# Kernel optimization log

Measured on AMD Instinct MI355X. Metric: run time of the kernel, lower is better.

The kernel has to match this reference:

```python
import jax, jax.numpy as jnp
import numpy as np

B, C, H, W = 32, 512, 64, 64
P = 8            # partition (window) size
HEAD_DIM = 32
N_HEADS = C // HEAD_DIM  # 16
MLP_RATIO = 4
LN_EPS = 1e-5


def _rel_pos_index(p):
    # Swin/MaxViT-style relative position index for a p x p window -> [p*p, p*p]
    coords = np.stack(np.meshgrid(np.arange(p), np.arange(p), indexing='ij'), 0).reshape(2, -1)
    rel = coords[:, :, None] - coords[:, None, :]          # [2, pp, pp]
    rel = rel.transpose(1, 2, 0) + (p - 1)                 # shift to >= 0
    idx = rel[..., 0] * (2 * p - 1) + rel[..., 1]          # [pp, pp]
    return jnp.asarray(idx, jnp.int32)


def setup_inputs() -> dict:
    key = jax.random.key(0)
    ks = jax.random.split(key, 10)
    s = 0.02
    d_ff = MLP_RATIO * C
    inp = {
        'x': jax.random.normal(ks[0], (B, C, H, W), jnp.float32),
        'gamma1': jnp.ones((C,), jnp.float32),
        'beta1': jnp.zeros((C,), jnp.float32),
        'gamma2': jnp.ones((C,), jnp.float32),
        'beta2': jnp.zeros((C,), jnp.float32),
        'qkv_w': jax.random.normal(ks[1], (C, 3 * C), jnp.float32) * s,
        'qkv_b': jnp.zeros((3 * C,), jnp.float32),
        'merge_w': jax.random.normal(ks[2], (C, C), jnp.float32) * s,
        'merge_b': jnp.zeros((C,), jnp.float32),
        'bias_table': jax.random.normal(ks[3], ((2 * P - 1) ** 2, N_HEADS), jnp.float32) * s,
        'w1': jax.random.normal(ks[4], (C, d_ff), jnp.float32) * s,
        'b1': jnp.zeros((d_ff,), jnp.float32),
        'w2': jax.random.normal(ks[5], (d_ff, C), jnp.float32) * s,
        'b2': jnp.zeros((C,), jnp.float32),
        'rel_idx': _rel_pos_index(P),
    }
    return inp


def _layernorm(t, g, b):
    mu = jnp.mean(t, axis=-1, keepdims=True)
    var = jnp.mean(jnp.square(t - mu), axis=-1, keepdims=True)
    return (t - mu) * jax.lax.rsqrt(var + LN_EPS) * g + b


def reference(x, gamma1, beta1, gamma2, beta2, qkv_w, qkv_b, merge_w, merge_b,
              bias_table, w1, b1, w2, b2, rel_idx):
    p, hd, nh = P, HEAD_DIM, N_HEADS
    Bx, Cx, Hx, Wx = x.shape
    hp, wp = Hx // p, Wx // p
    G, PP = hp * wp, p * p

    # --- window partition: [B,C,H,W] -> [B, G, p*p, C] (partition_type='window', no swap)
    xw = x.reshape(Bx, Cx, hp, p, wp, p).transpose(0, 2, 4, 3, 5, 1).reshape(Bx, G, PP, Cx)

    # --- relative-position multi-head attention on norm1(x)
    h = _layernorm(xw, gamma1, beta1)
    qkv = h @ qkv_w + qkv_b                                   # [B,G,PP,3C]
    q, k, v = jnp.split(qkv, 3, axis=-1)
    q = q.reshape(Bx, G, PP, nh, hd) * (hd ** -0.5)
    k = k.reshape(Bx, G, PP, nh, hd)
    v = v.reshape(Bx, G, PP, nh, hd)
    attn = jnp.einsum('bgqhd,bgkhd->bghqk', q, k)             # [B,G,nh,PP,PP]
    bias = bias_table[rel_idx]                                # [PP,PP,nh]
    attn = attn + bias.transpose(2, 0, 1)[None, None]
    attn = jax.nn.softmax(attn, axis=-1)
    o = jnp.einsum('bghqk,bgkhd->bgqhd', attn, v).reshape(Bx, G, PP, Cx)
    xw = xw + (o @ merge_w + merge_b)                          # residual (dropout/SD p=0)

    # --- MLP block on norm2(x)
    h2 = _layernorm(xw, gamma2, beta2)
    m = jax.nn.gelu(h2 @ w1 + b1) @ w2 + b2
    xw = xw + m

    # --- window departition: [B,G,p*p,C] -> [B,C,H,W]
    out = xw.reshape(Bx, hp, wp, p, p, Cx).transpose(0, 5, 1, 3, 2, 4).reshape(Bx, Cx, Hx, Wx)
    return out
```

## Files before the change

kernel.cpp:

```cpp
#include <hip/hip_runtime.h>
#include <stdint.h>

typedef __attribute__((ext_vector_type(8))) short short8;
typedef __attribute__((ext_vector_type(4))) float f32x4;
typedef __attribute__((address_space(3))) void lds_void;
typedef __attribute__((address_space(1))) void gv_void;

static __device__ __forceinline__ float bf2f(unsigned short u) {
    union { uint32_t i; float f; } v; v.i = ((uint32_t)u) << 16; return v.f;
}
static __device__ __forceinline__ unsigned short f2bf(float f) {
    union { float f; uint32_t i; } v; v.f = f;
    uint32_t i = v.i;
    uint32_t r = (i + 0x7fffu + ((i >> 16) & 1u)) >> 16;
    return (unsigned short)r;
}
static __device__ __forceinline__ float fexp(float x) {
    float r;
    asm("v_exp_f32 %0, %1" : "=v"(r) : "v"(x * 1.44269504088896f));
    return r;
}
static __device__ __forceinline__ float frcp(float x) {
    float r;
    asm("v_rcp_f32 %0, %1" : "=v"(r) : "v"(x));
    return r;
}

__global__ void k_detect(const void* __restrict__ g1, int* __restrict__ flag) {
    if (threadIdx.x == 0 && blockIdx.x == 0) {
        const unsigned short* u = (const unsigned short*)g1;
        flag[0] = (u[0] == 0x3F80u) ? 0 : 1;
    }
}

__global__ __launch_bounds__(256) void k_cvt(const void* __restrict__ src,
                                             unsigned short* __restrict__ dst,
                                             int n, const int* __restrict__ flag) {
    int i = blockIdx.x * 256 + threadIdx.x;
    if (i < n) {
        dst[i] = flag[0] ? f2bf(((const float*)src)[i])
                         : ((const unsigned short*)src)[i];
    }
}

__global__ __launch_bounds__(256) void k_transpose(const void* __restrict__ in,
                                                   unsigned short* __restrict__ out,
                                                   int R, int C, const int* __restrict__ flag) {
    __shared__ unsigned short tile[32][33];
    int isf = flag[0];
    int tx = threadIdx.x, ty = threadIdx.y;
    int x = blockIdx.x * 32 + tx;
    int y0 = blockIdx.y * 32;
    for (int j = ty; j < 32; j += 8) {
        size_t idx = (size_t)(y0 + j) * C + x;
        tile[j][tx] = isf ? f2bf(((const float*)in)[idx]) : ((const unsigned short*)in)[idx];
    }
    __syncthreads();
    int x2 = y0 + tx;
    int y20 = blockIdx.x * 32;
    for (int j = ty; j < 32; j += 8)
        out[(size_t)(y20 + j) * R + x2] = tile[tx][j];
}

__global__ __launch_bounds__(256) void k_prep_bias(const void* __restrict__ bias_table,
                                                   const int* __restrict__ rel_idx,
                                                   float* __restrict__ biasp,
                                                   const int* __restrict__ flag) {
    int i = blockIdx.x * 256 + threadIdx.x;
    int isf = flag[0];
    int h = i & 15, qk = i >> 4;
    size_t idx = (size_t)rel_idx[qk] * 16 + h;
    float v = isf ? ((const float*)bias_table)[idx] : bf2f(((const unsigned short*)bias_table)[idx]);
    biasp[h * 4096 + qk] = v;
}

__global__ __launch_bounds__(256) void k_partition_ln(const void* __restrict__ x,
                                                      const unsigned short* __restrict__ g1,
                                                      const unsigned short* __restrict__ b1,
                                                      unsigned short* __restrict__ xw,
                                                      unsigned short* __restrict__ h,
                                                      int b0, const int* __restrict__ flag) {
    __shared__ unsigned short tile[64][512];
    int isf = flag[0];
    int bh = blockIdx.x, bl = bh >> 6, hh = bh & 63;
    int b = b0 + bl;
    int tid = threadIdx.x;
    size_t xoff = (((size_t)b * 512) * 64 + hh) * 64;
    int c0 = tid >> 3, ch = tid & 7;
    if (isf) {
        const float* xb = (const float*)x + xoff;
        for (int k = 0; k < 16; ++k) {
            int c = c0 + k * 32;
            f32x4 v0 = *reinterpret_cast<const f32x4*>(xb + (size_t)c * 4096 + ch * 8);
            f32x4 v1 = *reinterpret_cast<const f32x4*>(xb + (size_t)c * 4096 + ch * 8 + 4);
#pragma unroll
            for (int j = 0; j < 4; ++j) tile[ch * 8 + j][c] = f2bf(v0[j]);
#pragma unroll
            for (int j = 0; j < 4; ++j) tile[ch * 8 + 4 + j][c] = f2bf(v1[j]);
        }
    } else {
        const unsigned short* xb = (const unsigned short*)x + xoff;
        for (int k = 0; k < 16; ++k) {
            int c = c0 + k * 32;
            short8 v = *reinterpret_cast<const short8*>(xb + (size_t)c * 4096 + ch * 8);
#pragma unroll
            for (int j = 0; j < 8; ++j) tile[ch * 8 + j][c] = (unsigned short)v[j];
        }
    }
    __syncthreads();
    int w = tid >> 2, q = tid & 3;
    float s = 0.f, s2 = 0.f;
#pragma unroll 4
    for (int j = 0; j < 128; ++j) {
        int c = q * 128 + ((j + 8 * w) & 127);
        float f = bf2f(tile[w][c]);
        s += f; s2 += f * f;
    }
    s += __shfl_xor(s, 1);  s += __shfl_xor(s, 2);
    s2 += __shfl_xor(s2, 1); s2 += __shfl_xor(s2, 2);
    float mu = s * (1.f / 512.f);
    float rstd = rsqrtf(s2 * (1.f / 512.f) - mu * mu + 1e-5f);
    int t = (bl * 64 + (hh >> 3) * 8 + (w >> 3)) * 64 + (hh & 7) * 8 + (w & 7);
    unsigned short* xr = xw + (size_t)t * 512;
    unsigned short* hr = h + (size_t)t * 512;
    for (int cc = q * 128; cc < q * 128 + 128; cc += 8) {
        short8 raw, hn;
#pragma unroll
        for (int j = 0; j < 8; ++j) {
            unsigned short u = tile[w][cc + j];
            raw[j] = (short)u;
            float f = (bf2f(u) - mu) * rstd * bf2f(g1[cc + j]) + bf2f(b1[cc + j]);
            hn[j] = (short)f2bf(f);
        }
        *reinterpret_cast<short8*>(xr + cc) = raw;
        *reinterpret_cast<short8*>(hr + cc) = hn;
    }
}

__global__ __launch_bounds__(256) void k_ln(const unsigned short* __restrict__ in,
                                            const unsigned short* __restrict__ g,
                                            const unsigned short* __restrict__ b,
                                            unsigned short* __restrict__ out) {
    int wid = threadIdx.x >> 6, lane = threadIdx.x & 63;
    size_t t = (size_t)blockIdx.x * 4 + wid;
    short8 v = *reinterpret_cast<const short8*>(in + t * 512 + lane * 8);
    float f[8], s = 0.f, s2 = 0.f;
#pragma unroll
    for (int j = 0; j < 8; ++j) { f[j] = bf2f((unsigned short)v[j]); s += f[j]; s2 += f[j] * f[j]; }
    for (int m = 1; m < 64; m <<= 1) { s += __shfl_xor(s, m); s2 += __shfl_xor(s2, m); }
    float mu = s * (1.f / 512.f);
    float rstd = rsqrtf(s2 * (1.f / 512.f) - mu * mu + 1e-5f);
    short8 ov;
#pragma unroll
    for (int j = 0; j < 8; ++j)
        ov[j] = (short)f2bf((f[j] - mu) * rstd * bf2f(g[lane * 8 + j]) + bf2f(b[lane * 8 + j]));
    *reinterpret_cast<short8*>(out + t * 512 + lane * 8) = ov;
}

template <int MODE>
__global__ __launch_bounds__(512, 1) void k_gemm5(const unsigned short* __restrict__ A,
                                                  const unsigned short* __restrict__ BT,
                                                  const unsigned short* __restrict__ bias,
                                                  const unsigned short* __restrict__ res,
                                                  unsigned short* __restrict__ out,
                                                  int M, int N, int K) {
    __shared__ unsigned short S[65536];
    const int tid = threadIdx.x, lane = tid & 63, wid = tid >> 6;

    int nwg = gridDim.x * gridDim.y;
    int lin = blockIdx.y * gridDim.x + blockIdx.x;
    int swz = (lin & 7) * (nwg >> 3) + (lin >> 3);
    int mt = swz % gridDim.x, nt = swz / gridDim.x;

    const int wr = wid >> 2, wc = wid & 3;
    const int rl = lane & 15, qg = lane >> 4;

    const int strow = tid >> 2;
    const int scb   = (tid & 3) ^ ((tid >> 3) & 3);
    const unsigned short* Agb = A  + ((size_t)mt * 256 + strow) * K + scb * 8;
    const unsigned short* Bgb = BT + ((size_t)nt * 256 + strow) * K + scb * 8;
    const int ldst = strow * 32 + (tid & 3) * 8;

    f32x4 acc[8][4];
#pragma unroll
    for (int mf = 0; mf < 8; ++mf)
#pragma unroll
        for (int nf = 0; nf < 4; ++nf) {
            acc[mf][nf][0] = 0.f; acc[mf][nf][1] = 0.f; acc[mf][nf][2] = 0.f; acc[mf][nf][3] = 0.f;
        }

    const int NH = K >> 5;

    auto stage = [&](int h) {
        int base = (h & 3) * 16384;
#pragma unroll
        for (int s = 0; s < 2; ++s) {
            __builtin_amdgcn_global_load_lds((const gv_void*)(Agb + (size_t)s * 128 * K + h * 32),
                                             (lds_void*)(&S[base + s * 4096 + ldst]), 16, 0, 0);
            __builtin_amdgcn_global_load_lds((const gv_void*)(Bgb + (size_t)s * 128 * K + h * 32),
                                             (lds_void*)(&S[base + 8192 + s * 4096 + ldst]), 16, 0, 0);
        }
    };

    stage(0); stage(1); stage(2);

    const int arow0 = wr * 128 + rl;
    const int brow0 = wc * 64 + rl;
    const int kbr = (qg ^ ((rl >> 1) & 3)) * 8;

    for (int h = 0; h < NH; ++h) {
        const unsigned short* sA = &S[(h & 3) * 16384];
        const unsigned short* sB = sA + 8192;
        if (h + 3 < NH) {
            stage(h + 3);
            asm volatile("s_waitcnt vmcnt(12)" ::: "memory");
        } else if (h + 2 < NH) {
            asm volatile("s_waitcnt vmcnt(8)" ::: "memory");
        } else if (h + 1 < NH) {
            asm volatile("s_waitcnt vmcnt(4)" ::: "memory");
        } else {
            asm volatile("s_waitcnt vmcnt(0)" ::: "memory");
        }
        __builtin_amdgcn_s_barrier();
        asm volatile("" ::: "memory");

        short8 af[8], bfr[4];
#pragma unroll
        for (int nf = 0; nf < 4; ++nf)
            bfr[nf] = *reinterpret_cast<const short8*>(&sB[(brow0 + nf * 16) * 32 + kbr]);
#pragma unroll
        for (int mf = 0; mf < 8; ++mf)
            af[mf] = *reinterpret_cast<const short8*>(&sA[(arow0 + mf * 16) * 32 + kbr]);

        __builtin_amdgcn_s_setprio(1);
#pragma unroll
        for (int mf = 0; mf < 8; ++mf)
#pragma unroll
            for (int nf = 0; nf < 4; ++nf)
                acc[mf][nf] = __builtin_amdgcn_mfma_f32_16x16x32_bf16(af[mf], bfr[nf], acc[mf][nf], 0, 0, 0);
        __builtin_amdgcn_s_setprio(0);

        __builtin_amdgcn_s_barrier();
        asm volatile("" ::: "memory");
    }

    const int PST = 264;
    unsigned short* pb = (unsigned short*)S;
    float bz[4];
#pragma unroll
    for (int nf = 0; nf < 4; ++nf) bz[nf] = bf2f(bias[nt * 256 + wc * 64 + nf * 16 + rl]);
    int row_l = tid >> 4, cbl = (tid & 15) * 16;
    int growb = mt * 256 + (row_l >> 4) * 128 + (row_l & 15);
    size_t gcol = (size_t)nt * 256 + cbl;

#pragma unroll
    for (int mf = 0; mf < 8; ++mf) {
        __syncthreads();
#pragma unroll
        for (int nf = 0; nf < 4; ++nf)
#pragma unroll
            for (int r = 0; r < 4; ++r) {
                float v = acc[mf][nf][r] + bz[nf];
                if (MODE == 2) {
                    float z = 0.7978845608f * (v + 0.044715f * v * v * v);
                    float e = fexp(-2.0f * z);
                    v = v * frcp(1.f + e);
                }
                pb[(wr * 16 + qg * 4 + r) * PST + wc * 64 + nf * 16 + rl] = f2bf(v);
            }
        __syncthreads();
        size_t go = (size_t)(growb + mf * 16) * N + gcol;
        short8 o1 = *reinterpret_cast<const short8*>(&pb[row_l * PST + cbl]);
        short8 o2 = *reinterpret_cast<const short8*>(&pb[row_l * PST + cbl + 8]);
        if (MODE == 1) {
            short8 r1 = *reinterpret_cast<const short8*>(&res[go]);
            short8 r2 = *reinterpret_cast<const short8*>(&res[go + 8]);
#pragma unroll
            for (int j = 0; j < 8; ++j) {
                o1[j] = (short)f2bf(bf2f((unsigned short)o1[j]) + bf2f((unsigned short)r1[j]));
                o2[j] = (short)f2bf(bf2f((unsigned short)o2[j]) + bf2f((unsigned short)r2[j]));
            }
        }
        *reinterpret_cast<short8*>(&out[go]) = o1;
        *reinterpret_cast<short8*>(&out[go + 8]) = o2;
    }
}

__global__ __launch_bounds__(64) void k_attn(const unsigned short* __restrict__ qkv,
                                             const float* __restrict__ biasp,
                                             unsigned short* __restrict__ o) {
    __shared__ unsigned short Pl[64][72];
    int blk = blockIdx.x;
    int head = blk & 15, win = blk >> 4;
    size_t T0 = (size_t)win * 64;
    int lane = threadIdx.x;
    int rl = lane & 15, qg = lane >> 4;
    const unsigned short* base = qkv + T0 * 1536;
    int qoff = head * 32, koff = 512 + head * 32, voff = 1024 + head * 32;

    f32x4 s[4][4];
#pragma unroll
    for (int m = 0; m < 4; ++m)
#pragma unroll
        for (int n = 0; n < 4; ++n) { s[m][n][0] = 0.f; s[m][n][1] = 0.f; s[m][n][2] = 0.f; s[m][n][3] = 0.f; }

    short8 aq[4], bk[4];
#pragma unroll
    for (int m = 0; m < 4; ++m)
        aq[m] = *reinterpret_cast<const short8*>(base + (size_t)(16 * m + rl) * 1536 + qoff + qg * 8);
#pragma unroll
    for (int n = 0; n < 4; ++n)
        bk[n] = *reinterpret_cast<const short8*>(base + (size_t)(16 * n + rl) * 1536 + koff + qg * 8);
#pragma unroll
    for (int m = 0; m < 4; ++m)
#pragma unroll
        for (int n = 0; n < 4; ++n)
            s[m][n] = __builtin_amdgcn_mfma_f32_16x16x32_bf16(aq[m], bk[n], s[m][n], 0, 0, 0);

    const float scale = 0.17677669529663687f;
    const float* bh = biasp + head * 4096;
#pragma unroll
    for (int m = 0; m < 4; ++m) {
#pragma unroll
        for (int r = 0; r < 4; ++r) {
            int row = 16 * m + qg * 4 + r;
            float v0 = s[m][0][r] * scale + bh[row * 64 + rl];
            float v1 = s[m][1][r] * scale + bh[row * 64 + 16 + rl];
            float v2 = s[m][2][r] * scale + bh[row * 64 + 32 + rl];
            float v3 = s[m][3][r] * scale + bh[row * 64 + 48 + rl];
            float mx = fmaxf(fmaxf(v0, v1), fmaxf(v2, v3));
            mx = fmaxf(mx, __shfl_xor(mx, 1));
            mx = fmaxf(mx, __shfl_xor(mx, 2));
            mx = fmaxf(mx, __shfl_xor(mx, 4));
            mx = fmaxf(mx, __shfl_xor(mx, 8));
            v0 = fexp(v0 - mx); v1 = fexp(v1 - mx); v2 = fexp(v2 - mx); v3 = fexp(v3 - mx);
            float sm = v0 + v1 + v2 + v3;
            sm += __shfl_xor(sm, 1);
            sm += __shfl_xor(sm, 2);
            sm += __shfl_xor(sm, 4);
            sm += __shfl_xor(sm, 8);
            float inv = frcp(sm);
            Pl[row][rl]      = f2bf(v0 * inv);
            Pl[row][16 + rl] = f2bf(v1 * inv);
            Pl[row][32 + rl] = f2bf(v2 * inv);
            Pl[row][48 + rl] = f2bf(v3 * inv);
        }
    }
    __syncthreads();

    short8 bv[2][2];
#pragma unroll
    for (int ks = 0; ks < 2; ++ks)
#pragma unroll
        for (int n2 = 0; n2 < 2; ++n2) {
            short8 t;
#pragma unroll
            for (int i = 0; i < 8; ++i)
                t[i] = (short)base[(size_t)(32 * ks + qg * 8 + i) * 1536 + voff + n2 * 16 + rl];
            bv[ks][n2] = t;
        }

    f32x4 acc2[4][2];
#pragma unroll
    for (int m = 0; m < 4; ++m)
#pragma unroll
        for (int n2 = 0; n2 < 2; ++n2) { acc2[m][n2][0] = 0.f; acc2[m][n2][1] = 0.f; acc2[m][n2][2] = 0.f; acc2[m][n2][3] = 0.f; }

#pragma unroll
    for (int m = 0; m < 4; ++m) {
        short8 p0 = *reinterpret_cast<const short8*>(&Pl[16 * m + rl][qg * 8]);
        short8 p1 = *reinterpret_cast<const short8*>(&Pl[16 * m + rl][32 + qg * 8]);
#pragma unroll
        for (int n2 = 0; n2 < 2; ++n2) {
            acc2[m][n2] = __builtin_amdgcn_mfma_f32_16x16x32_bf16(p0, bv[0][n2], acc2[m][n2], 0, 0, 0);
            acc2[m][n2] = __builtin_amdgcn_mfma_f32_16x16x32_bf16(p1, bv[1][n2], acc2[m][n2], 0, 0, 0);
        }
    }
#pragma unroll
    for (int m = 0; m < 4; ++m)
#pragma unroll
        for (int n2 = 0; n2 < 2; ++n2)
#pragma unroll
            for (int r = 0; r < 4; ++r) {
                int row = 16 * m + qg * 4 + r;
                o[(T0 + row) * 512 + head * 32 + n2 * 16 + rl] = f2bf(acc2[m][n2][r]);
            }
}

__global__ __launch_bounds__(256) void k_departition(const unsigned short* __restrict__ tok,
                                                     void* __restrict__ xo,
                                                     int b0, const int* __restrict__ flag) {
    __shared__ unsigned short tile[64][512];
    int isf = flag[0];
    int bh = blockIdx.x, bl = bh >> 6, hh = bh & 63;
    int b = b0 + bl;
    int tid = threadIdx.x;
    int Tb = (bl * 64 + (hh >> 3) * 8) * 64 + (hh & 7) * 8;
    for (int k = 0; k < 16; ++k) {
        int flat = k * 256 + tid;
        int w = flat >> 6, ch = flat & 63;
        int t = Tb + (w >> 3) * 64 + (w & 7);
        short8 v = *reinterpret_cast<const short8*>(tok + (size_t)t * 512 + ch * 8);
        *reinterpret_cast<short8*>(&tile[w][ch * 8]) = v;
    }
    __syncthreads();
    size_t xoff = (((size_t)b * 512) * 64 + hh) * 64;
    if (isf) {
        float* xb = (float*)xo + xoff;
        for (int k = 0; k < 16; ++k) {
            int flat = k * 256 + tid;
            int c = flat >> 3, wc = flat & 7;
            f32x4 a, d;
#pragma unroll
            for (int j = 0; j < 4; ++j) a[j] = bf2f(tile[wc * 8 + j][c]);
#pragma unroll
            for (int j = 0; j < 4; ++j) d[j] = bf2f(tile[wc * 8 + 4 + j][c]);
            *reinterpret_cast<f32x4*>(xb + (size_t)c * 4096 + wc * 8) = a;
            *reinterpret_cast<f32x4*>(xb + (size_t)c * 4096 + wc * 8 + 4) = d;
        }
    } else {
        unsigned short* xb = (unsigned short*)xo + xoff;
        for (int k = 0; k < 16; ++k) {
            int flat = k * 256 + tid;
            int c = flat >> 3, wc = flat & 7;
            short8 v;
#pragma unroll
            for (int j = 0; j < 8; ++j) v[j] = (short)tile[wc * 8 + j][c];
            *reinterpret_cast<short8*>(xb + (size_t)c * 4096 + wc * 8) = v;
        }
    }
}

extern "C" void kernel_launch(void* const* d_in, const int* in_sizes, int n_in,
                              void* d_out, int out_size, void* d_ws, size_t ws_size,
                              hipStream_t stream) {
    const void* x          = d_in[0];
    const void* g1         = d_in[1];
    const void* be1        = d_in[2];
    const void* g2         = d_in[3];
    const void* be2        = d_in[4];
    const void* qkv_w      = d_in[5];
    const void* qkv_b      = d_in[6];
    const void* merge_w    = d_in[7];
    const void* merge_b    = d_in[8];
    const void* bias_table = d_in[9];
    const void* w1         = d_in[10];
    const void* b1         = d_in[11];
    const void* w2         = d_in[12];
    const void* b2         = d_in[13];
    const int*  rel_idx    = (const int*)d_in[14];

    const size_t extra = 8u << 20;
    int CB = 4;
    if (ws_size >= (size_t)32768 * 10240 + extra) CB = 8;
    int nch = 32 / CB;
    size_t tok = (size_t)CB * 4096;

    unsigned short* xw_c     = (unsigned short*)d_ws;
    unsigned short* h_c      = xw_c + tok * 512;
    unsigned short* o_c      = h_c + tok * 512;
    unsigned short* qkv_c    = o_c + tok * 512;
    unsigned short* mid_c    = qkv_c + tok * 1536;
    unsigned short* qkv_wT   = mid_c + tok * 2048;
    unsigned short* merge_wT = qkv_wT + 1536 * 512;
    unsigned short* w1T      = merge_wT + 512 * 512;
    unsigned short* w2T      = w1T + 2048 * 512;
    unsigned short* vecs     = w2T + 512 * 2048;
    float*          biasp    = (float*)(vecs + 6656);
    int*            flag     = (int*)(biasp + 65536);

    unsigned short* ng1 = vecs + 0,    *nbe1 = vecs + 512;
    unsigned short* ng2 = vecs + 1024, *nbe2 = vecs + 1536;
    unsigned short* nqb = vecs + 2048, *nmb  = vecs + 3584;
    unsigned short* nb1 = vecs + 4096, *nb2  = vecs + 6144;

    k_detect<<<1, 64, 0, stream>>>(g1, flag);
    k_cvt<<<2, 256, 0, stream>>>(g1, ng1, 512, flag);
    k_cvt<<<2, 256, 0, stream>>>(be1, nbe1, 512, flag);
    k_cvt<<<2, 256, 0, stream>>>(g2, ng2, 512, flag);
    k_cvt<<<2, 256, 0, stream>>>(be2, nbe2, 512, flag);
    k_cvt<<<6, 256, 0, stream>>>(qkv_b, nqb, 1536, flag);
    k_cvt<<<2, 256, 0, stream>>>(merge_b, nmb, 512, flag);
    k_cvt<<<8, 256, 0, stream>>>(b1, nb1, 2048, flag);
    k_cvt<<<2, 256, 0, stream>>>(b2, nb2, 512, flag);
    k_transpose<<<dim3(48, 16), dim3(32, 8), 0, stream>>>(qkv_w, qkv_wT, 512, 1536, flag);
    k_transpose<<<dim3(16, 16), dim3(32, 8), 0, stream>>>(merge_w, merge_wT, 512, 512, flag);
    k_transpose<<<dim3(64, 16), dim3(32, 8), 0, stream>>>(w1, w1T, 512, 2048, flag);
    k_transpose<<<dim3(16, 64), dim3(32, 8), 0, stream>>>(w2, w2T, 2048, 512, flag);
    k_prep_bias<<<256, 256, 0, stream>>>(bias_table, rel_idx, biasp, flag);

    int mtiles = (int)(tok / 256);
    int M = (int)tok;
    for (int c = 0; c < nch; ++c) {
        int b0 = c * CB;
        k_partition_ln<<<CB * 64, 256, 0, stream>>>(x, ng1, nbe1, xw_c, h_c, b0, flag);
        k_gemm5<0><<<dim3(mtiles, 6), 512, 0, stream>>>(h_c, qkv_wT, nqb, nullptr, qkv_c, M, 1536, 512);
        k_attn<<<CB * 1024, 64, 0, stream>>>(qkv_c, biasp, o_c);
        k_gemm5<1><<<dim3(mtiles, 2), 512, 0, stream>>>(o_c, merge_wT, nmb, xw_c, xw_c, M, 512, 512);
        k_ln<<<(int)(tok / 4), 256, 0, stream>>>(xw_c, ng2, nbe2, h_c);
        k_gemm5<2><<<dim3(mtiles, 8), 512, 0, stream>>>(h_c, w1T, nb1, nullptr, mid_c, M, 2048, 512);
        k_gemm5<1><<<dim3(mtiles, 2), 512, 0, stream>>>(mid_c, w2T, nb2, xw_c, qkv_c, M, 512, 2048);
        k_departition<<<CB * 64, 256, 0, stream>>>(qkv_c, d_out, b0, flag);
    }
}
```

Baseline: 1.870 ms.

## Fuse departition into FFN2 epilogue and emit transposed V from QKV GEMM

Measured after the change: 1.964 ms. +5.0%, slower.

```diff
diff --git a/kernel.cpp b/kernel.cpp
--- a/kernel.cpp
+++ b/kernel.cpp
@@ -23,6 +23,11 @@
 static __device__ __forceinline__ float frcp(float x) {
     float r;
     asm("v_rcp_f32 %0, %1" : "=v"(r) : "v"(x));
+    return r;
+}
+static __device__ __forceinline__ uint32_t cvtpk(float lo, float hi) {
+    uint32_t r;
+    asm("v_cvt_pk_bf16_f32 %0, %1, %2" : "=v"(r) : "v"(lo), "v"(hi));
     return r;
 }
 
@@ -64,14 +69,16 @@
 
 __global__ __launch_bounds__(256) void k_prep_bias(const void* __restrict__ bias_table,
                                                    const int* __restrict__ rel_idx,
-                                                   float* __restrict__ biasp,
+                                                   float* __restrict__ biasb,
                                                    const int* __restrict__ flag) {
     int i = blockIdx.x * 256 + threadIdx.x;
     int isf = flag[0];
-    int h = i & 15, qk = i >> 4;
-    size_t idx = (size_t)rel_idx[qk] * 16 + h;
+    int r  = i & 3, rl = (i >> 2) & 15, qg = (i >> 6) & 3;
+    int km = (i >> 8) & 3, qn = (i >> 10) & 3, h = (i >> 12) & 15;
+    int q = 16 * qn + rl, k = 16 * km + 4 * qg + r;
+    size_t idx = (size_t)rel_idx[q * 64 + k] * 16 + h;
     float v = isf ? ((const float*)bias_table)[idx] : bf2f(((const unsigned short*)bias_table)[idx]);
-    biasp[h * 4096 + qk] = v;
+    biasb[i] = v;
 }
 
 __global__ __launch_bounds__(256) void k_partition_ln(const void* __restrict__ x,
@@ -158,11 +165,14 @@
 }
 
 template <int MODE>
-__global__ __launch_bounds__(512, 1) void k_gemm5(const unsigned short* __restrict__ A,
+__global__ __launch_bounds__(512, 1) void k_gemm6(const unsigned short* __restrict__ A,
                                                   const unsigned short* __restrict__ BT,
                                                   const unsigned short* __restrict__ bias,
                                                   const unsigned short* __restrict__ res,
                                                   unsigned short* __restrict__ out,
+                                                  unsigned short* __restrict__ vt,
+                                                  void* __restrict__ outx,
+                                                  int b0, const int* __restrict__ flag,
                                                   int M, int N, int K) {
     __shared__ unsigned short S[65536];
     const int tid = threadIdx.x, lane = tid & 63, wid = tid >> 6;
@@ -252,6 +262,7 @@
     int row_l = tid >> 4, cbl = (tid & 15) * 16;
     int growb = mt * 256 + (row_l >> 4) * 128 + (row_l & 15);
     size_t gcol = (size_t)nt * 256 + cbl;
+    const int isf = (MODE == 3) ? flag[0] : 0;
 
 #pragma unroll
     for (int mf = 0; mf < 8; ++mf) {
@@ -266,169 +277,170 @@
                     float e = fexp(-2.0f * z);
                     v = v * frcp(1.f + e);
                 }
+                if (MODE == 3) {
+                    size_t rowg = (size_t)(mt * 256 + wr * 128 + mf * 16 + qg * 4 + r);
+                    v += bf2f(res[rowg * N + nt * 256 + wc * 64 + nf * 16 + rl]);
+                }
                 pb[(wr * 16 + qg * 4 + r) * PST + wc * 64 + nf * 16 + rl] = f2bf(v);
             }
         __syncthreads();
-        size_t go = (size_t)(growb + mf * 16) * N + gcol;
-        short8 o1 = *reinterpret_cast<const short8*>(&pb[row_l * PST + cbl]);
-        short8 o2 = *reinterpret_cast<const short8*>(&pb[row_l * PST + cbl + 8]);
-        if (MODE == 1) {
-            short8 r1 = *reinterpret_cast<const short8*>(&res[go]);
-            short8 r2 = *reinterpret_cast<const short8*>(&res[go + 8]);
-#pragma unroll
-            for (int j = 0; j < 8; ++j) {
-                o1[j] = (short)f2bf(bf2f((unsigned short)o1[j]) + bf2f((unsigned short)r1[j]));
-                o2[j] = (short)f2bf(bf2f((unsigned short)o2[j]) + bf2f((unsigned short)r2[j]));
+
+        if (MODE == 0 && nt >= 4) {
+#pragma unroll
+            for (int s = 0; s < 2; ++s) {
+                int run = tid + 512 * s;
+                int c = run & 255, hp = run >> 8, half = hp >> 1, ph = hp & 1;
+                int prow = half * 16 + ph * 8;
+                short8 v8;
+#pragma unroll
+                for (int i = 0; i < 8; ++i) v8[i] = (short)pb[(prow + i) * PST + c];
+                int t0 = mt * 256 + half * 128 + mf * 16 + ph * 8;
+                int cc = nt * 256 + c - 1024;
+                int win = t0 >> 6, k0 = t0 & 63;
+                *reinterpret_cast<short8*>(&vt[((size_t)(win * 16 + (cc >> 5)) * 32 + (cc & 31)) * 64 + k0]) = v8;
             }
-        }
-        *reinterpret_cast<short8*>(&out[go]) = o1;
-        *reinterpret_cast<short8*>(&out[go + 8]) = o2;
-    }
-}
-
-__global__ __launch_bounds__(64) void k_attn(const unsigned short* __restrict__ qkv,
-                                             const float* __restrict__ biasp,
-                                             unsigned short* __restrict__ o) {
-    __shared__ unsigned short Pl[64][72];
+        } else if (MODE == 3) {
+#pragma unroll
+            for (int s = 0; s < 2; ++s) {
+                int run = tid + 512 * s;
+                int c = run & 255, hp = run >> 8, half = hp >> 1, ph = hp & 1;
+                int prow = half * 16 + ph * 8;
+                int t0 = mt * 256 + half * 128 + mf * 16 + ph * 8;
+                int ch = nt * 256 + c;
+                int b = b0 + (t0 >> 12), win = (t0 >> 6) & 63, py = (t0 >> 3) & 7;
+                size_t xoff = ((size_t)(b * 512 + ch)) * 4096 + ((win >> 3) * 8 + py) * 64 + (win & 7) * 8;
+                if (isf) {
+                    f32x4 a, d;
+#pragma unroll
+                    for (int i = 0; i < 4; ++i) a[i] = bf2f(pb[(prow + i) * PST + c]);
+#pragma unroll
+                    for (int i = 0; i < 4; ++i) d[i] = bf2f(pb[(prow + 4 + i) * PST + c]);
+                    *reinterpret_cast<f32x4*>((float*)outx + xoff) = a;
+                    *reinterpret_cast<f32x4*>((float*)outx + xoff + 4) = d;
+                } else {
+                    short8 v8;
+#pragma unroll
+                    for (int i = 0; i < 8; ++i) v8[i] = (short)pb[(prow + i) * PST + c];
+                    *reinterpret_cast<short8*>((unsigned short*)outx + xoff) = v8;
+                }
+            }
+        } else {
+            size_t go = (size_t)(growb + mf * 16) * N + gcol;
+            short8 o1 = *reinterpret_cast<const short8*>(&pb[row_l * PST + cbl]);
+            short8 o2 = *reinterpret_cast<const short8*>(&pb[row_l * PST + cbl + 8]);
+            if (MODE == 1) {
+                short8 r1 = *reinterpret_cast<const short8*>(&res[go]);
+                short8 r2 = *reinterpret_cast<const short8*>(&res[go + 8]);
+#pragma unroll
+                for (int j = 0; j < 8; ++j) {
+                    o1[j] = (short)f2bf(bf2f((unsigned short)o1[j]) + bf2f((unsigned short)r1[j]));
+                    o2[j] = (short)f2bf(bf2f((unsigned short)o2[j]) + bf2f((unsigned short)r2[j]));
+                }
+            }
+            *reinterpret_cast<short8*>(&out[go]) = o1;
+            *reinterpret_cast<short8*>(&out[go + 8]) = o2;
+        }
+    }
+}
+
+__global__ __launch_bounds__(64) void k_attn2(const unsigned short* __restrict__ qkv,
+                                              const unsigned short* __restrict__ vt,
+                                              const float* __restrict__ biasb,
+                                              unsigned short* __restrict__ o) {
+    __shared__ unsigned short Pl[64 * 72];
     int blk = blockIdx.x;
     int head = blk & 15, win = blk >> 4;
     size_t T0 = (size_t)win * 64;
     int lane = threadIdx.x;
     int rl = lane & 15, qg = lane >> 4;
     const unsigned short* base = qkv + T0 * 1536;
-    int qoff = head * 32, koff = 512 + head * 32, voff = 1024 + head * 32;
-
-    f32x4 s[4][4];
-#pragma unroll
-    for (int m = 0; m < 4; ++m)
-#pragma unroll
-        for (int n = 0; n < 4; ++n) { s[m][n][0] = 0.f; s[m][n][1] = 0.f; s[m][n][2] = 0.f; s[m][n][3] = 0.f; }
-
-    short8 aq[4], bk[4];
-#pragma unroll
-    for (int m = 0; m < 4; ++m)
-        aq[m] = *reinterpret_cast<const short8*>(base + (size_t)(16 * m + rl) * 1536 + qoff + qg * 8);
-#pragma unroll
-    for (int n = 0; n < 4; ++n)
-        bk[n] = *reinterpret_cast<const short8*>(base + (size_t)(16 * n + rl) * 1536 + koff + qg * 8);
-#pragma unroll
-    for (int m = 0; m < 4; ++m)
-#pragma unroll
-        for (int n = 0; n < 4; ++n)
-            s[m][n] = __builtin_amdgcn_mfma_f32_16x16x32_bf16(aq[m], bk[n], s[m][n], 0, 0, 0);
+    int qoff = head * 32, koff = 512 + head * 32;
+
+    short8 kf[4], qf[4];
+#pragma unroll
+    for (int m = 0; m < 4; ++m) {
+        kf[m] = *reinterpret_cast<const short8*>(base + (size_t)(16 * m + rl) * 1536 + koff + qg * 8);
+        qf[m] = *reinterpret_cast<const short8*>(base + (size_t)(16 * m + rl) * 1536 + qoff + qg * 8);
+    }
+    f32x4 st[4][4];
+#pragma unroll
+    for (int km = 0; km < 4; ++km)
+#pragma unroll
+        for (int qn = 0; qn < 4; ++qn) { st[km][qn][0] = 0.f; st[km][qn][1] = 0.f; st[km][qn][2] = 0.f; st[km][qn][3] = 0.f; }
+#pragma unroll
+    for (int km = 0; km < 4; ++km)
+#pragma unroll
+        for (int qn = 0; qn < 4; ++qn)
+            st[km][qn] = __builtin_amdgcn_mfma_f32_16x16x32_bf16(kf[km], qf[qn], st[km][qn], 0, 0, 0);
 
     const float scale = 0.17677669529663687f;
-    const float* bh = biasp + head * 4096;
-#pragma unroll
-    for (int m = 0; m < 4; ++m) {
-#pragma unroll
-        for (int r = 0; r < 4; ++r) {
-            int row = 16 * m + qg * 4 + r;
-            float v0 = s[m][0][r] * scale + bh[row * 64 + rl];
-            float v1 = s[m][1][r] * scale + bh[row * 64 + 16 + rl];
-            float v2 = s[m][2][r] * scale + bh[row * 64 + 32 + rl];
-            float v3 = s[m][3][r] * scale + bh[row * 64 + 48 + rl];
-            float mx = fmaxf(fmaxf(v0, v1), fmaxf(v2, v3));
-            mx = fmaxf(mx, __shfl_xor(mx, 1));
-            mx = fmaxf(mx, __shfl_xor(mx, 2));
-            mx = fmaxf(mx, __shfl_xor(mx, 4));
-            mx = fmaxf(mx, __shfl_xor(mx, 8));
-            v0 = fexp(v0 - mx); v1 = fexp(v1 - mx); v2 = fexp(v2 - mx); v3 = fexp(v3 - mx);
-            float sm = v0 + v1 + v2 + v3;
-            sm += __shfl_xor(sm, 1);
-            sm += __shfl_xor(sm, 2);
-            sm += __shfl_xor(sm, 4);
-            sm += __shfl_xor(sm, 8);
-            float inv = frcp(sm);
-            Pl[row][rl]      = f2bf(v0 * inv);
-            Pl[row][16 + rl] = f2bf(v1 * inv);
-            Pl[row][32 + rl] = f2bf(v2 * inv);
-            Pl[row][48 + rl] = f2bf(v3 * inv);
-        }
-    }
+    const float* bh = biasb + head * 4096 + qg * 64 + rl * 4;
+#pragma unroll
+    for (int qn = 0; qn < 4; ++qn) {
+        float vv[4][4];
+        float mx = -3.0e38f;
+#pragma unroll
+        for (int km = 0; km < 4; ++km) {
+            f32x4 b4 = *reinterpret_cast<const f32x4*>(bh + qn * 1024 + km * 256);
+#pragma unroll
+            for (int r = 0; r < 4; ++r) {
+                vv[km][r] = st[km][qn][r] * scale + b4[r];
+                mx = fmaxf(mx, vv[km][r]);
+            }
+        }
+        mx = fmaxf(mx, __shfl_xor(mx, 16));
+        mx = fmaxf(mx, __shfl_xor(mx, 32));
+        float sm = 0.f;
+#pragma unroll
+        for (int km = 0; km < 4; ++km)
+#pragma unroll
+            for (int r = 0; r < 4; ++r) { vv[km][r] = fexp(vv[km][r] - mx); sm += vv[km][r]; }
+        sm += __shfl_xor(sm, 16);
+        sm += __shfl_xor(sm, 32);
+        float inv = frcp(sm);
+        int q = 16 * qn + rl;
+#pragma unroll
+        for (int km = 0; km < 4; ++km) {
+            uint32_t w0 = cvtpk(vv[km][0] * inv, vv[km][1] * inv);
+            uint32_t w1 = cvtpk(vv[km][2] * inv, vv[km][3] * inv);
+            uint32_t* p = reinterpret_cast<uint32_t*>(&Pl[q * 72 + 16 * km + 4 * qg]);
+            p[0] = w0; p[1] = w1;
+        }
+    }
+
+    short8 vf[2][2];
+    const unsigned short* vb = vt + (size_t)(win * 16 + head) * 2048;
+#pragma unroll
+    for (int kb = 0; kb < 2; ++kb)
+#pragma unroll
+        for (int dn = 0; dn < 2; ++dn)
+            vf[kb][dn] = *reinterpret_cast<const short8*>(vb + (16 * dn + rl) * 64 + 32 * kb + 8 * qg);
+
     __syncthreads();
 
-    short8 bv[2][2];
-#pragma unroll
-    for (int ks = 0; ks < 2; ++ks)
-#pragma unroll
-        for (int n2 = 0; n2 < 2; ++n2) {
-            short8 t;
-#pragma unroll
-            for (int i = 0; i < 8; ++i)
-                t[i] = (short)base[(size_t)(32 * ks + qg * 8 + i) * 1536 + voff + n2 * 16 + rl];
-            bv[ks][n2] = t;
-        }
-
-    f32x4 acc2[4][2];
-#pragma unroll
-    for (int m = 0; m < 4; ++m)
-#pragma unroll
-        for (int n2 = 0; n2 < 2; ++n2) { acc2[m][n2][0] = 0.f; acc2[m][n2][1] = 0.f; acc2[m][n2][2] = 0.f; acc2[m][n2][3] = 0.f; }
-
-#pragma unroll
-    for (int m = 0; m < 4; ++m) {
-        short8 p0 = *reinterpret_cast<const short8*>(&Pl[16 * m + rl][qg * 8]);
-        short8 p1 = *reinterpret_cast<const short8*>(&Pl[16 * m + rl][32 + qg * 8]);
-#pragma unroll
-        for (int n2 = 0; n2 < 2; ++n2) {
-            acc2[m][n2] = __builtin_amdgcn_mfma_f32_16x16x32_bf16(p0, bv[0][n2], acc2[m][n2], 0, 0, 0);
-            acc2[m][n2] = __builtin_amdgcn_mfma_f32_16x16x32_bf16(p1, bv[1][n2], acc2[m][n2], 0, 0, 0);
-        }
-    }
-#pragma unroll
-    for (int m = 0; m < 4; ++m)
-#pragma unroll
-        for (int n2 = 0; n2 < 2; ++n2)
-#pragma unroll
-            for (int r = 0; r < 4; ++r) {
-                int row = 16 * m + qg * 4 + r;
-                o[(T0 + row) * 512 + head * 32 + n2 * 16 + rl] = f2bf(acc2[m][n2][r]);
-            }
-}
-
-__global__ __launch_bounds__(256) void k_departition(const unsigned short* __restrict__ tok,
-                                                     void* __restrict__ xo,
-                                                     int b0, const int* __restrict__ flag) {
-    __shared__ unsigned short tile[64][512];
-    int isf = flag[0];
-    int bh = blockIdx.x, bl = bh >> 6, hh = bh & 63;
-    int b = b0 + bl;
-    int tid = threadIdx.x;
-    int Tb = (bl * 64 + (hh >> 3) * 8) * 64 + (hh & 7) * 8;
-    for (int k = 0; k < 16; ++k) {
-        int flat = k * 256 + tid;
-        int w = flat >> 6, ch = flat & 63;
-        int t = Tb + (w >> 3) * 64 + (w & 7);
-        short8 v = *reinterpret_cast<const short8*>(tok + (size_t)t * 512 + ch * 8);
-        *reinterpret_cast<short8*>(&tile[w][ch * 8]) = v;
-    }
-    __syncthreads();
-    size_t xoff = (((size_t)b * 512) * 64 + hh) * 64;
-    if (isf) {
-        float* xb = (float*)xo + xoff;
-        for (int k = 0; k < 16; ++k) {
-            int flat = k * 256 + tid;
-            int c = flat >> 3, wc = flat & 7;
-            f32x4 a, d;
-#pragma unroll
-            for (int j = 0; j < 4; ++j) a[j] = bf2f(tile[wc * 8 + j][c]);
-#pragma unroll
-            for (int j = 0; j < 4; ++j) d[j] = bf2f(tile[wc * 8 + 4 + j][c]);
-            *reinterpret_cast<f32x4*>(xb + (size_t)c * 4096 + wc * 8) = a;
-            *reinterpret_cast<f32x4*>(xb + (size_t)c * 4096 + wc * 8 + 4) = d;
-        }
-    } else {
-        unsigned short* xb = (unsigned short*)xo + xoff;
-        for (int k = 0; k < 16; ++k) {
-            int flat = k * 256 + tid;
-            int c = flat >> 3, wc = flat & 7;
-            short8 v;
-#pragma unroll
-            for (int j = 0; j < 8; ++j) v[j] = (short)tile[wc * 8 + j][c];
-            *reinterpret_cast<short8*>(xb + (size_t)c * 4096 + wc * 8) = v;
-        }
-    }
+    f32x4 acc[4][2];
+#pragma unroll
+    for (int qm = 0; qm < 4; ++qm)
+#pragma unroll
+        for (int dn = 0; dn < 2; ++dn) { acc[qm][dn][0] = 0.f; acc[qm][dn][1] = 0.f; acc[qm][dn][2] = 0.f; acc[qm][dn][3] = 0.f; }
+
+#pragma unroll
+    for (int qm = 0; qm < 4; ++qm) {
+        short8 a0 = *reinterpret_cast<const short8*>(&Pl[(16 * qm + rl) * 72 + 8 * qg]);
+        short8 a1 = *reinterpret_cast<const short8*>(&Pl[(16 * qm + rl) * 72 + 32 + 8 * qg]);
+#pragma unroll
+        for (int dn = 0; dn < 2; ++dn) {
+            acc[qm][dn] = __builtin_amdgcn_mfma_f32_16x16x32_bf16(a0, vf[0][dn], acc[qm][dn], 0, 0, 0);
+            acc[qm][dn] = __builtin_amdgcn_mfma_f32_16x16x32_bf16(a1, vf[1][dn], acc[qm][dn], 0, 0, 0);
+        }
+    }
+#pragma unroll
+    for (int qm = 0; qm < 4; ++qm)
+#pragma unroll
+        for (int dn = 0; dn < 2; ++dn)
+#pragma unroll
+            for (int r = 0; r < 4; ++r)
+                o[(T0 + 16 * qm + 4 * qg + r) * 512 + head * 32 + 16 * dn + rl] = f2bf(acc[qm][dn][r]);
 }
 
 extern "C" void kernel_launch(void* const* d_in, const int* in_sizes, int n_in,
@@ -452,7 +464,7 @@
 
     const size_t extra = 8u << 20;
     int CB = 4;
-    if (ws_size >= (size_t)32768 * 10240 + extra) CB = 8;
+    if (ws_size >= (size_t)32768 * 11264 + extra) CB = 8;
     int nch = 32 / CB;
     size_t tok = (size_t)CB * 4096;
 
@@ -461,13 +473,14 @@
     unsigned short* o_c      = h_c + tok * 512;
     unsigned short* qkv_c    = o_c + tok * 512;
     unsigned short* mid_c    = qkv_c + tok * 1536;
-    unsigned short* qkv_wT   = mid_c + tok * 2048;
+    unsigned short* vt_c     = mid_c + tok * 2048;
+    unsigned short* qkv_wT   = vt_c + tok * 512;
     unsigned short* merge_wT = qkv_wT + 1536 * 512;
     unsigned short* w1T      = merge_wT + 512 * 512;
     unsigned short* w2T      = w1T + 2048 * 512;
     unsigned short* vecs     = w2T + 512 * 2048;
-    float*          biasp    = (float*)(vecs + 6656);
-    int*            flag     = (int*)(biasp + 65536);
+    float*          biasb    = (float*)(vecs + 6656);
+    int*            flag     = (int*)(biasb + 65536);
 
     unsigned short* ng1 = vecs + 0,    *nbe1 = vecs + 512;
     unsigned short* ng2 = vecs + 1024, *nbe2 = vecs + 1536;
@@ -487,19 +500,22 @@
     k_transpose<<<dim3(16, 16), dim3(32, 8), 0, stream>>>(merge_w, merge_wT, 512, 512, flag);
     k_transpose<<<dim3(64, 16), dim3(32, 8), 0, stream>>>(w1, w1T, 512, 2048, flag);
     k_transpose<<<dim3(16, 64), dim3(32, 8), 0, stream>>>(w2, w2T, 2048, 512, flag);
-    k_prep_bias<<<256, 256, 0, stream>>>(bias_table, rel_idx, biasp, flag);
+    k_prep_bias<<<256, 256, 0, stream>>>(bias_table, rel_idx, biasb, flag);
 
     int mtiles = (int)(tok / 256);
     int M = (int)tok;
     for (int c = 0; c < nch; ++c) {
         int b0 = c * CB;
         k_partition_ln<<<CB * 64, 256, 0, stream>>>(x, ng1, nbe1, xw_c, h_c, b0, flag);
-        k_gemm5<0><<<dim3(mtiles, 6), 512, 0, stream>>>(h_c, qkv_wT, nqb, nullptr, qkv_c, M, 1536, 512);
-        k_attn<<<CB * 1024, 64, 0, stream>>>(qkv_c, biasp, o_c);
-        k_gemm5<1><<<dim3(mtiles, 2), 512, 0, stream>>>(o_c, merge_wT, nmb, xw_c, xw_c, M, 512, 512);
+        k_gemm6<0><<<dim3(mtiles, 6), 512, 0, stream>>>(h_c, qkv_wT, nqb, nullptr, qkv_c, vt_c,
+                                                        nullptr, 0, flag, M, 1536, 512);
+        k_attn2<<<CB * 1024, 64, 0, stream>>>(qkv_c, vt_c, biasb, o_c);
+        k_gemm6<1><<<dim3(mtiles, 2), 512, 0, stream>>>(o_c, merge_wT, nmb, xw_c, xw_c, nullptr,
+                                                        nullptr, 0, flag, M, 512, 512);
         k_ln<<<(int)(tok / 4), 256, 0, stream>>>(xw_c, ng2, nbe2, h_c);
-        k_gemm5<2><<<dim3(mtiles, 8), 512, 0, stream>>>(h_c, w1T, nb1, nullptr, mid_c, M, 2048, 512);
-        k_gemm5<1><<<dim3(mtiles, 2), 512, 0, stream>>>(mid_c, w2T, nb2, xw_c, qkv_c, M, 512, 2048);
-        k_departition<<<CB * 64, 256, 0, stream>>>(qkv_c, d_out, b0, flag);
-    }
-}
+        k_gemm6<2><<<dim3(mtiles, 8), 512, 0, stream>>>(h_c, w1T, nb1, nullptr, mid_c, nullptr,
+                                                        nullptr, 0, flag, M, 2048, 512);
+        k_gemm6<3><<<dim3(mtiles, 2), 512, 0, stream>>>(mid_c, w2T, nb2, xw_c, qkv_c, nullptr,
+                                                        d_out, b0, flag, M, 512, 2048);
+    }
+}
```

## Widen GEMM epilogue stores and stage V in LDS across four heads per attention block

Applied to the files above, without the earlier changes.

Measured after the change: 2.016 ms. 1.08x slower.

```diff
diff --git a/kernel.cpp b/kernel.cpp
--- a/kernel.cpp
+++ b/kernel.cpp
@@ -158,12 +158,12 @@
 }
 
 template <int MODE>
-__global__ __launch_bounds__(512, 1) void k_gemm5(const unsigned short* __restrict__ A,
-                                                  const unsigned short* __restrict__ BT,
-                                                  const unsigned short* __restrict__ bias,
-                                                  const unsigned short* __restrict__ res,
-                                                  unsigned short* __restrict__ out,
-                                                  int M, int N, int K) {
+__global__ __launch_bounds__(512, 1) void k_gemm10(const unsigned short* __restrict__ A,
+                                                   const unsigned short* __restrict__ BT,
+                                                   const unsigned short* __restrict__ bias,
+                                                   const unsigned short* __restrict__ res,
+                                                   unsigned short* __restrict__ out,
+                                                   int M, int N, int K) {
     __shared__ unsigned short S[65536];
     const int tid = threadIdx.x, lane = tid & 63, wid = tid >> 6;
 
@@ -249,74 +249,115 @@
     float bz[4];
 #pragma unroll
     for (int nf = 0; nf < 4; ++nf) bz[nf] = bf2f(bias[nt * 256 + wc * 64 + nf * 16 + rl]);
-    int row_l = tid >> 4, cbl = (tid & 15) * 16;
-    int growb = mt * 256 + (row_l >> 4) * 128 + (row_l & 15);
-    size_t gcol = (size_t)nt * 256 + cbl;
-
-#pragma unroll
-    for (int mf = 0; mf < 8; ++mf) {
+    const int row_l = tid >> 3;
+    const int cof   = (tid & 7) * 32;
+    const int wrr = row_l >> 5, jj = (row_l >> 4) & 1, sub = row_l & 15;
+
+#pragma unroll
+    for (int mp = 0; mp < 4; ++mp) {
         __syncthreads();
 #pragma unroll
-        for (int nf = 0; nf < 4; ++nf)
-#pragma unroll
-            for (int r = 0; r < 4; ++r) {
-                float v = acc[mf][nf][r] + bz[nf];
-                if (MODE == 2) {
-                    float z = 0.7978845608f * (v + 0.044715f * v * v * v);
-                    float e = fexp(-2.0f * z);
-                    v = v * frcp(1.f + e);
+        for (int j = 0; j < 2; ++j) {
+            int mf = mp * 2 + j;
+#pragma unroll
+            for (int nf = 0; nf < 4; ++nf)
+#pragma unroll
+                for (int r = 0; r < 4; ++r) {
+                    float v = acc[mf][nf][r] + bz[nf];
+                    if (MODE == 2) {
+                        float z = 0.7978845608f * (v + 0.044715f * v * v * v);
+                        float e = fexp(-2.0f * z);
+                        v = v * frcp(1.f + e);
+                    }
+                    pb[(wr * 32 + j * 16 + qg * 4 + r) * PST + wc * 64 + nf * 16 + rl] = f2bf(v);
                 }
-                pb[(wr * 16 + qg * 4 + r) * PST + wc * 64 + nf * 16 + rl] = f2bf(v);
-            }
+        }
         __syncthreads();
-        size_t go = (size_t)(growb + mf * 16) * N + gcol;
-        short8 o1 = *reinterpret_cast<const short8*>(&pb[row_l * PST + cbl]);
-        short8 o2 = *reinterpret_cast<const short8*>(&pb[row_l * PST + cbl + 8]);
+        int grow = mt * 256 + wrr * 128 + (mp * 2 + jj) * 16 + sub;
+        size_t go = (size_t)grow * N + nt * 256 + cof;
+        short8 o1 = *reinterpret_cast<const short8*>(&pb[row_l * PST + cof]);
+        short8 o2 = *reinterpret_cast<const short8*>(&pb[row_l * PST + cof + 8]);
+        short8 o3 = *reinterpret_cast<const short8*>(&pb[row_l * PST + cof + 16]);
+        short8 o4 = *reinterpret_cast<const short8*>(&pb[row_l * PST + cof + 24]);
         if (MODE == 1) {
             short8 r1 = *reinterpret_cast<const short8*>(&res[go]);
             short8 r2 = *reinterpret_cast<const short8*>(&res[go + 8]);
+            short8 r3 = *reinterpret_cast<const short8*>(&res[go + 16]);
+            short8 r4 = *reinterpret_cast<const short8*>(&res[go + 24]);
 #pragma unroll
             for (int j = 0; j < 8; ++j) {
                 o1[j] = (short)f2bf(bf2f((unsigned short)o1[j]) + bf2f((unsigned short)r1[j]));
                 o2[j] = (short)f2bf(bf2f((unsigned short)o2[j]) + bf2f((unsigned short)r2[j]));
+                o3[j] = (short)f2bf(bf2f((unsigned short)o3[j]) + bf2f((unsigned short)r3[j]));
+                o4[j] = (short)f2bf(bf2f((unsigned short)o4[j]) + bf2f((unsigned short)r4[j]));
             }
         }
-        *reinterpret_cast<short8*>(&out[go]) = o1;
-        *reinterpret_cast<short8*>(&out[go + 8]) = o2;
-    }
-}
-
-__global__ __launch_bounds__(64) void k_attn(const unsigned short* __restrict__ qkv,
-                                             const float* __restrict__ biasp,
-                                             unsigned short* __restrict__ o) {
-    __shared__ unsigned short Pl[64][72];
+        *reinterpret_cast<short8*>(&out[go])      = o1;
+        *reinterpret_cast<short8*>(&out[go + 8])  = o2;
+        *reinterpret_cast<short8*>(&out[go + 16]) = o3;
+        *reinterpret_cast<short8*>(&out[go + 24]) = o4;
+    }
+}
+
+__global__ __launch_bounds__(256) void k_attn3(const unsigned short* __restrict__ qkv,
+                                               const float* __restrict__ biasp,
+                                               unsigned short* __restrict__ o) {
+    __shared__ unsigned short S[4 * 64 * 72];
     int blk = blockIdx.x;
-    int head = blk & 15, win = blk >> 4;
+    int hq = blk & 3, win = blk >> 2;
     size_t T0 = (size_t)win * 64;
-    int lane = threadIdx.x;
+    int tid = threadIdx.x, lane = tid & 63, wid = tid >> 6;
     int rl = lane & 15, qg = lane >> 4;
+    int head = hq * 4 + wid;
     const unsigned short* base = qkv + T0 * 1536;
-    int qoff = head * 32, koff = 512 + head * 32, voff = 1024 + head * 32;
+    int qoff = head * 32, koff = 512 + head * 32, voff = 1024 + hq * 128;
+
+    unsigned short* Vl = S;
+    {
+        int r0 = tid >> 4, cb = (tid & 15) * 8;
+#pragma unroll
+        for (int it = 0; it < 4; ++it) {
+            int row = r0 + it * 16;
+            short8 v = *reinterpret_cast<const short8*>(base + (size_t)row * 1536 + voff + cb);
+            *reinterpret_cast<short8*>(&Vl[row * 136 + cb]) = v;
+        }
+    }
+
+    short8 aq[4], bk[4];
+#pragma unroll
+    for (int m = 0; m < 4; ++m) {
+        aq[m] = *reinterpret_cast<const short8*>(base + (size_t)(16 * m + rl) * 1536 + qoff + qg * 8);
+        bk[m] = *reinterpret_cast<const short8*>(base + (size_t)(16 * m + rl) * 1536 + koff + qg * 8);
+    }
 
     f32x4 s[4][4];
 #pragma unroll
     for (int m = 0; m < 4; ++m)
 #pragma unroll
         for (int n = 0; n < 4; ++n) { s[m][n][0] = 0.f; s[m][n][1] = 0.f; s[m][n][2] = 0.f; s[m][n][3] = 0.f; }
-
-    short8 aq[4], bk[4];
-#pragma unroll
-    for (int m = 0; m < 4; ++m)
-        aq[m] = *reinterpret_cast<const short8*>(base + (size_t)(16 * m + rl) * 1536 + qoff + qg * 8);
-#pragma unroll
-    for (int n = 0; n < 4; ++n)
-        bk[n] = *reinterpret_cast<const short8*>(base + (size_t)(16 * n + rl) * 1536 + koff + qg * 8);
 #pragma unroll
     for (int m = 0; m < 4; ++m)
 #pragma unroll
         for (int n = 0; n < 4; ++n)
             s[m][n] = __builtin_amdgcn_mfma_f32_16x16x32_bf16(aq[m], bk[n], s[m][n], 0, 0, 0);
 
+    __syncthreads();
+
+    short8 bv[2][2];
+#pragma unroll
+    for (int ks = 0; ks < 2; ++ks)
+#pragma unroll
+        for (int n2 = 0; n2 < 2; ++n2) {
+            short8 t;
+#pragma unroll
+            for (int i = 0; i < 8; ++i)
+                t[i] = (short)Vl[(32 * ks + qg * 8 + i) * 136 + wid * 32 + n2 * 16 + rl];
+            bv[ks][n2] = t;
+        }
+
+    __syncthreads();
+
+    unsigned short* Pl = S + wid * (64 * 72);
     const float scale = 0.17677669529663687f;
     const float* bh = biasp + head * 4096;
 #pragma unroll
@@ -340,25 +381,12 @@
             sm += __shfl_xor(sm, 4);
             sm += __shfl_xor(sm, 8);
             float inv = frcp(sm);
-            Pl[row][rl]      = f2bf(v0 * inv);
-            Pl[row][16 + rl] = f2bf(v1 * inv);
-            Pl[row][32 + rl] = f2bf(v2 * inv);
-            Pl[row][48 + rl] = f2bf(v3 * inv);
-        }
-    }
-    __syncthreads();
-
-    short8 bv[2][2];
-#pragma unroll
-    for (int ks = 0; ks < 2; ++ks)
-#pragma unroll
-        for (int n2 = 0; n2 < 2; ++n2) {
-            short8 t;
-#pragma unroll
-            for (int i = 0; i < 8; ++i)
-                t[i] = (short)base[(size_t)(32 * ks + qg * 8 + i) * 1536 + voff + n2 * 16 + rl];
-            bv[ks][n2] = t;
-        }
+            Pl[row * 72 + rl]      = f2bf(v0 * inv);
+            Pl[row * 72 + 16 + rl] = f2bf(v1 * inv);
+            Pl[row * 72 + 32 + rl] = f2bf(v2 * inv);
+            Pl[row * 72 + 48 + rl] = f2bf(v3 * inv);
+        }
+    }
 
     f32x4 acc2[4][2];
 #pragma unroll
@@ -368,8 +396,8 @@
 
 #pragma unroll
     for (int m = 0; m < 4; ++m) {
-        short8 p0 = *reinterpret_cast<const short8*>(&Pl[16 * m + rl][qg * 8]);
-        short8 p1 = *reinterpret_cast<const short8*>(&Pl[16 * m + rl][32 + qg * 8]);
+        short8 p0 = *reinterpret_cast<const short8*>(&Pl[(16 * m + rl) * 72 + qg * 8]);
+        short8 p1 = *reinterpret_cast<const short8*>(&Pl[(16 * m + rl) * 72 + 32 + qg * 8]);
 #pragma unroll
         for (int n2 = 0; n2 < 2; ++n2) {
             acc2[m][n2] = __builtin_amdgcn_mfma_f32_16x16x32_bf16(p0, bv[0][n2], acc2[m][n2], 0, 0, 0);
@@ -494,12 +522,12 @@
     for (int c = 0; c < nch; ++c) {
         int b0 = c * CB;
         k_partition_ln<<<CB * 64, 256, 0, stream>>>(x, ng1, nbe1, xw_c, h_c, b0, flag);
-        k_gemm5<0><<<dim3(mtiles, 6), 512, 0, stream>>>(h_c, qkv_wT, nqb, nullptr, qkv_c, M, 1536, 512);
-        k_attn<<<CB * 1024, 64, 0, stream>>>(qkv_c, biasp, o_c);
-        k_gemm5<1><<<dim3(mtiles, 2), 512, 0, stream>>>(o_c, merge_wT, nmb, xw_c, xw_c, M, 512, 512);
+        k_gemm10<0><<<dim3(mtiles, 6), 512, 0, stream>>>(h_c, qkv_wT, nqb, nullptr, qkv_c, M, 1536, 512);
+        k_attn3<<<CB * 256, 256, 0, stream>>>(qkv_c, biasp, o_c);
+        k_gemm10<1><<<dim3(mtiles, 2), 512, 0, stream>>>(o_c, merge_wT, nmb, xw_c, xw_c, M, 512, 512);
         k_ln<<<(int)(tok / 4), 256, 0, stream>>>(xw_c, ng2, nbe2, h_c);
-        k_gemm5<2><<<dim3(mtiles, 8), 512, 0, stream>>>(h_c, w1T, nb1, nullptr, mid_c, M, 2048, 512);
-        k_gemm5<1><<<dim3(mtiles, 2), 512, 0, stream>>>(mid_c, w2T, nb2, xw_c, qkv_c, M, 512, 2048);
+        k_gemm10<2><<<dim3(mtiles, 8), 512, 0, stream>>>(h_c, w1T, nb1, nullptr, mid_c, M, 2048, 512);
+        k_gemm10<1><<<dim3(mtiles, 2), 512, 0, stream>>>(mid_c, w2T, nb2, xw_c, qkv_c, M, 512, 2048);
         k_departition<<<CB * 64, 256, 0, stream>>>(qkv_c, d_out, b0, flag);
     }
 }
```
